# Kernel tuning notes

Measured on AMD Instinct MI355X. Metric: run time of the kernel, lower is better.

The kernel has to match this reference:

```python
import jax, jax.numpy as jnp
import numpy as np

D_MODEL = 1024
D_INNER = 2048   # expand_factor * d_model
D_STATE = 16
D_CONV = 4
DT_RANK = 64     # ceil(d_model / 16)
EPS = 1e-5


def setup_inputs() -> dict:
    key = jax.random.key(0)
    ks = jax.random.split(key, 10)
    B, L = 2, 1024
    w = lambda k, shape, s: (jax.random.normal(k, shape, jnp.float32) * s)
    A = jnp.tile(jnp.arange(1, D_STATE + 1, dtype=jnp.float32), (D_INNER, 1))
    return {
        "hidden_states": jax.random.normal(ks[0], (B, L, D_MODEL), jnp.float32),
        "norm_w": jnp.ones((D_MODEL,), jnp.float32),
        "norm_b": jnp.zeros((D_MODEL,), jnp.float32),
        "in_proj_w": w(ks[1], (D_MODEL, 2 * D_INNER), 0.02),
        "conv_w": w(ks[2], (D_INNER, D_CONV), 0.2),
        "conv_b": jnp.zeros((D_INNER,), jnp.float32),
        "x_proj_w": w(ks[3], (D_INNER, DT_RANK + 2 * D_STATE), 0.02),
        "dt_proj_w": w(ks[4], (DT_RANK, D_INNER), 0.1),
        "dt_proj_b": w(ks[5], (D_INNER,), 0.1),
        "A_log": jnp.log(A),
        "D_param": jnp.ones((D_INNER,), jnp.float32),
        "out_proj_w": w(ks[6], (D_INNER, D_MODEL), 0.02),
    }


def _causal_depthwise_conv(x, conv_w, conv_b):
    # x: [B, L, d_inner] -> causal depthwise conv, kernel size D_CONV
    B, L, C = x.shape
    xt = jnp.transpose(x, (0, 2, 1))                 # [B, C, L]
    xt = jnp.pad(xt, ((0, 0), (0, 0), (D_CONV - 1, 0)))  # left pad == torch pad+truncate
    k = conv_w[:, None, :]                            # [C, 1, K] (OIH, groups=C)
    y = jax.lax.conv_general_dilated(
        xt, k, window_strides=(1,), padding="VALID",
        dimension_numbers=("NCH", "OIH", "NCH"), feature_group_count=C)
    y = y + conv_b[None, :, None]
    return jnp.transpose(y, (0, 2, 1))                # [B, L, C]


def _selective_scan(u, delta, A, Bm, Cm, D_param):
    # u, delta: [B, L, d_inner]; A: [d_inner, d_state]; Bm, Cm: [B, L, d_state]
    dA = jnp.exp(delta[..., None] * A[None, None])            # [B,L,d,n]
    dBu = delta[..., None] * Bm[:, :, None, :] * u[..., None]  # [B,L,d,n]
    h0 = jnp.zeros((u.shape[0], u.shape[2], A.shape[1]), u.dtype)

    def step(h, inp):
        dA_t, dBu_t, c_t = inp          # [B,d,n], [B,d,n], [B,n]
        h = dA_t * h + dBu_t
        y = jnp.einsum("bdn,bn->bd", h, c_t)
        return h, y

    xs = (jnp.moveaxis(dA, 1, 0), jnp.moveaxis(dBu, 1, 0), jnp.moveaxis(Cm, 1, 0))
    _, ys = jax.lax.scan(step, h0, xs)   # ys: [L, B, d]
    y = jnp.moveaxis(ys, 0, 1)           # [B, L, d]
    return y + u * D_param[None, None]


def reference(hidden_states, norm_w, norm_b, in_proj_w, conv_w, conv_b,
              x_proj_w, dt_proj_w, dt_proj_b, A_log, D_param, out_proj_w):
    h = hidden_states
    mu = jnp.mean(h, axis=-1, keepdims=True)
    var = jnp.mean(jnp.square(h - mu), axis=-1, keepdims=True)
    h = (h - mu) * jax.lax.rsqrt(var + EPS) * norm_w + norm_b

    xz = h @ in_proj_w                       # [B,L,2*d_inner]
    x, z = jnp.split(xz, 2, axis=-1)
    x = _causal_depthwise_conv(x, conv_w, conv_b)
    x = jax.nn.silu(x)

    A = -jnp.exp(A_log)                      # [d_inner, d_state]
    xp = x @ x_proj_w                        # [B,L,dt_rank+2*d_state]
    dt_r = xp[..., :DT_RANK]
    Bm = xp[..., DT_RANK:DT_RANK + D_STATE]
    Cm = xp[..., DT_RANK + D_STATE:]
    delta = jax.nn.softplus(dt_r @ dt_proj_w + dt_proj_b)  # [B,L,d_inner]

    y = _selective_scan(x, delta, A, Bm, Cm, D_param)
    y = y * jax.nn.silu(z)
    return y @ out_proj_w
```

## Files before the change

kernel.cpp:

```cpp
#include <hip/hip_runtime.h>
#include <hip/hip_bf16.h>

#define D_MODEL 1024
#define D_INNER 2048
#define D_STATE 16
#define DT_RANK 64
#define NB 2
#define LSEQ 1024
#define NROWS (NB * LSEQ)
#define XPN 96
#define NC 32
#define CL 32

typedef __attribute__((ext_vector_type(8))) short bf16x8;
typedef __attribute__((ext_vector_type(4))) float f32x4;

__device__ __forceinline__ unsigned short f2bf(float x) {
    __hip_bfloat16 h = __float2bfloat16(x);
    return *reinterpret_cast<unsigned short*>(&h);
}
__device__ __forceinline__ float bf2f(unsigned short u) {
    unsigned int v = ((unsigned int)u) << 16;
    float f;
    __builtin_memcpy(&f, &v, 4);
    return f;
}
__device__ __forceinline__ unsigned short f2h(float x) {
    _Float16 h = (_Float16)x;
    unsigned short u;
    __builtin_memcpy(&u, &h, 2);
    return u;
}
__device__ __forceinline__ float h2f(unsigned short u) {
    _Float16 h;
    __builtin_memcpy(&h, &u, 2);
    return (float)h;
}

__global__ __launch_bounds__(256) void wcast_ln(const float* __restrict__ W0, unsigned short* __restrict__ D0,
                                                const float* __restrict__ W1, unsigned short* __restrict__ D1,
                                                const float* __restrict__ W2, unsigned short* __restrict__ D2,
                                                const float* __restrict__ W3, unsigned short* __restrict__ D3,
                                                const float* __restrict__ hx, const float* __restrict__ nw,
                                                const float* __restrict__ nb, unsigned short* __restrict__ lnout) {
    int bid = blockIdx.x;
    if (bid >= 6528) {
        int row = bid - 6528;
        const float4* xr = (const float4*)(hx + (size_t)row * D_MODEL);
        float4 v = xr[threadIdx.x];
        float s = v.x + v.y + v.z + v.w;
        float sq = v.x * v.x + v.y * v.y + v.z * v.z + v.w * v.w;
#pragma unroll
        for (int off = 32; off > 0; off >>= 1) {
            s += __shfl_down(s, off);
            sq += __shfl_down(sq, off);
        }
        __shared__ float ws[4], wq[4];
        __shared__ float smu, srstd;
        int wave = threadIdx.x >> 6;
        if ((threadIdx.x & 63) == 0) { ws[wave] = s; wq[wave] = sq; }
        __syncthreads();
        if (threadIdx.x == 0) {
            float ts = ws[0] + ws[1] + ws[2] + ws[3];
            float tq = wq[0] + wq[1] + wq[2] + wq[3];
            float mu = ts * (1.f / D_MODEL);
            float var = tq * (1.f / D_MODEL) - mu * mu;
            smu = mu;
            srstd = rsqrtf(var + 1e-5f);
        }
        __syncthreads();
        float mu = smu, rstd = srstd;
        float4 wv = ((const float4*)nw)[threadIdx.x];
        float4 bv = ((const float4*)nb)[threadIdx.x];
        ushort4 pk;
        pk.x = f2bf((v.x - mu) * rstd * wv.x + bv.x);
        pk.y = f2bf((v.y - mu) * rstd * wv.y + bv.y);
        pk.z = f2bf((v.z - mu) * rstd * wv.z + bv.z);
        pk.w = f2bf((v.w - mu) * rstd * wv.w + bv.w);
        *(ushort4*)(lnout + (size_t)row * D_MODEL + threadIdx.x * 4) = pk;
        return;
    }
    const float* W;
    unsigned short* Dst;
    int K, Nreal, bx, by;
    if (bid < 4096) { W = W0; Dst = D0; K = 1024; Nreal = 4096; bx = bid & 127; by = bid >> 7; }
    else if (bid < 4352) { int j = bid - 4096; W = W1; Dst = D1; K = 2048; Nreal = 96; bx = j & 3; by = j >> 2; }
    else if (bid < 6400) { int j = bid - 4352; W = W2; Dst = D2; K = 2048; Nreal = 1024; bx = j & 31; by = j >> 5; }
    else { int j = bid - 6400; W = W3; Dst = D3; K = 64; Nreal = 2048; bx = j & 63; by = j >> 6; }
    __shared__ float t[32][33];
    int tn = bx * 32, tk = by * 32;
    for (int e = threadIdx.x; e < 1024; e += 256) {
        int r = e >> 5, c = e & 31;
        int n = tn + c;
        t[r][c] = (n < Nreal) ? W[(size_t)(tk + r) * Nreal + n] : 0.f;
    }
    __syncthreads();
    for (int e = threadIdx.x; e < 1024; e += 256) {
        int r = e >> 5, c = e & 31;
        Dst[(size_t)(tn + r) * K + tk + c] = f2bf(t[c][r]);
    }
}

template <int EPI>
__global__ __launch_bounds__(256) void gemm_bf16(const unsigned short* __restrict__ A,
                                                 const unsigned short* __restrict__ Bt,
                                                 const float* __restrict__ bias,
                                                 float* __restrict__ C,
                                                 void* __restrict__ C2,
                                                 int M, int K, int ldc, int Nreal) {
    __shared__ unsigned short As[128 * 64];
    __shared__ unsigned short Bs[128 * 64];
    int nwg = gridDim.x * gridDim.y;
    int orig = blockIdx.y * gridDim.x + blockIdx.x;
    int q = nwg >> 3, r = nwg & 7;
    int xcd = orig & 7, idx = orig >> 3;
    int newid = (xcd < r ? xcd * (q + 1) : r * (q + 1) + (xcd - r) * q) + idx;
    int bx = newid % gridDim.x, by = newid / gridDim.x;

    int tid = threadIdx.x;
    int lane = tid & 63;
    int wave = tid >> 6;
    int wr = (wave >> 1) * 64, wc = (wave & 1) * 64;
    int bm = by * 128, bn = bx * 128;
    int kchunk = K / gridDim.z;
    int kbeg = blockIdx.z * kchunk;

    f32x4 acc[4][4];
#pragma unroll
    for (int i = 0; i < 4; ++i)
#pragma unroll
        for (int j = 0; j < 4; ++j) acc[i][j] = (f32x4){0.f, 0.f, 0.f, 0.f};

    int ar = lane & 15;
    int kq = lane >> 4;

    for (int k0 = kbeg; k0 < kbeg + kchunk; k0 += 64) {
        __syncthreads();
#pragma unroll
        for (int s = 0; s < 4; ++s) {
            int seg = s * 256 + tid;
            int row = seg >> 3, p = seg & 7;
            int c = p ^ (row & 7);
            __builtin_amdgcn_global_load_lds(
                (const __attribute__((address_space(1))) void*)(A + (size_t)(bm + row) * K + k0 + c * 8),
                (__attribute__((address_space(3))) void*)(As + seg * 8), 16, 0, 0);
        }
#pragma unroll
        for (int s = 0; s < 4; ++s) {
            int seg = s * 256 + tid;
            int row = seg >> 3, p = seg & 7;
            int c = p ^ (row & 7);
            __builtin_amdgcn_global_load_lds(
                (const __attribute__((address_space(1))) void*)(Bt + (size_t)(bn + row) * K + k0 + c * 8),
                (__attribute__((address_space(3))) void*)(Bs + seg * 8), 16, 0, 0);
        }
        __syncthreads();
#pragma unroll
        for (int kk = 0; kk < 2; ++kk) {
            bf16x8 af[4], bfr[4];
#pragma unroll
            for (int i = 0; i < 4; ++i) {
                int row = wr + i * 16 + ar;
                int pos = ((kk << 2) | kq) ^ (row & 7);
                af[i] = *(const bf16x8*)&As[(size_t)row * 64 + pos * 8];
            }
#pragma unroll
            for (int j = 0; j < 4; ++j) {
                int row = wc + j * 16 + ar;
                int pos = ((kk << 2) | kq) ^ (row & 7);
                bfr[j] = *(const bf16x8*)&Bs[(size_t)row * 64 + pos * 8];
            }
#pragma unroll
            for (int i = 0; i < 4; ++i)
#pragma unroll
                for (int j = 0; j < 4; ++j)
                    acc[i][j] = __builtin_amdgcn_mfma_f32_16x16x32_bf16(af[i], bfr[j], acc[i][j], 0, 0, 0);
        }
    }

    int crow0 = bm + wr + (lane >> 4) * 4;
    int ccol0 = bn + wc + (lane & 15);
    size_t zoff = (size_t)blockIdx.z * (size_t)M * ldc;
#pragma unroll
    for (int i = 0; i < 4; ++i)
#pragma unroll
        for (int j = 0; j < 4; ++j) {
            int col = ccol0 + j * 16;
            if (EPI == 0) {
                if (col < Nreal) {
                    float* cp = C + zoff + (size_t)(crow0 + i * 16) * ldc + col;
#pragma unroll
                    for (int rr = 0; rr < 4; ++rr) cp[(size_t)rr * ldc] = acc[i][j][rr];
                }
            } else if (EPI == 2) {
                unsigned short* cx = (unsigned short*)C;
                unsigned short* cz = (unsigned short*)C2;
                if (col < 2048) {
#pragma unroll
                    for (int rr = 0; rr < 4; ++rr)
                        cx[(size_t)(crow0 + i * 16 + rr) * 2048 + col] = f2bf(acc[i][j][rr]);
                } else {
#pragma unroll
                    for (int rr = 0; rr < 4; ++rr)
                        cz[(size_t)(crow0 + i * 16 + rr) * 2048 + (col - 2048)] = f2bf(acc[i][j][rr]);
                }
            } else if (EPI == 3) {
                unsigned short* cp = (unsigned short*)C2 + zoff + (size_t)(crow0 + i * 16) * ldc + col;
#pragma unroll
                for (int rr = 0; rr < 4; ++rr) cp[(size_t)rr * ldc] = f2h(acc[i][j][rr]);
            } else {
                float bv = bias[col];
                unsigned short* cp = (unsigned short*)C2 + (size_t)(crow0 + i * 16) * ldc + col;
#pragma unroll
                for (int rr = 0; rr < 4; ++rr) {
                    float v = acc[i][j][rr] + bv;
                    v = (v > 20.f) ? v : log1pf(__expf(v));
                    cp[(size_t)rr * ldc] = f2bf(v);
                }
            }
        }
}

__global__ __launch_bounds__(256) void reduce_xp(const float* __restrict__ part,
                                                 float* __restrict__ xp,
                                                 unsigned short* __restrict__ dtr) {
    int t = blockIdx.x * 256 + threadIdx.x;
    float s = 0.f;
#pragma unroll
    for (int k = 0; k < 16; ++k) s += part[(size_t)k * ((size_t)NROWS * XPN) + t];
    xp[t] = s;
    int row = t / 96, col = t - row * 96;
    if (col < 64) dtr[(size_t)row * 64 + col] = f2bf(s);
}

__global__ __launch_bounds__(256) void reduce_out(const unsigned short* __restrict__ part,
                                                  float* __restrict__ out) {
    int t = blockIdx.x * 256 + threadIdx.x;
    const size_t stride = (size_t)NROWS * D_MODEL;
    ushort4 p0 = ((const ushort4*)part)[t];
    ushort4 p1 = ((const ushort4*)(part + stride))[t];
    ushort4 p2 = ((const ushort4*)(part + 2 * stride))[t];
    ushort4 p3 = ((const ushort4*)(part + 3 * stride))[t];
    float4 o;
    o.x = h2f(p0.x) + h2f(p1.x) + h2f(p2.x) + h2f(p3.x);
    o.y = h2f(p0.y) + h2f(p1.y) + h2f(p2.y) + h2f(p3.y);
    o.z = h2f(p0.z) + h2f(p1.z) + h2f(p2.z) + h2f(p3.z);
    o.w = h2f(p0.w) + h2f(p1.w) + h2f(p2.w) + h2f(p3.w);
    ((float4*)out)[t] = o;
}

__global__ __launch_bounds__(256) void conv_silu_kernel(const unsigned short* __restrict__ xx,
                                                        const float* __restrict__ cw,
                                                        const float* __restrict__ cb,
                                                        unsigned short* __restrict__ outb) {
    int gid = blockIdx.x * 256 + threadIdx.x;
    int d4 = (gid & 511) << 2;
    int bl = gid >> 9;
    int l = bl & (LSEQ - 1);
    const unsigned short* base = xx + (size_t)bl * D_INNER + d4;
    ushort4 zr4 = {0, 0, 0, 0};
    ushort4 X0 = *(const ushort4*)base;
    ushort4 X1 = (l >= 1) ? *(const ushort4*)(base - D_INNER) : zr4;
    ushort4 X2 = (l >= 2) ? *(const ushort4*)(base - 2 * D_INNER) : zr4;
    ushort4 X3 = (l >= 3) ? *(const ushort4*)(base - 3 * D_INNER) : zr4;
    float4 bias = *(const float4*)(cb + d4);
    const float4* wv = (const float4*)(cw + (size_t)d4 * 4);
    float xs0[4] = {bf2f(X0.x), bf2f(X0.y), bf2f(X0.z), bf2f(X0.w)};
    float xs1[4] = {bf2f(X1.x), bf2f(X1.y), bf2f(X1.z), bf2f(X1.w)};
    float xs2[4] = {bf2f(X2.x), bf2f(X2.y), bf2f(X2.z), bf2f(X2.w)};
    float xs3[4] = {bf2f(X3.x), bf2f(X3.y), bf2f(X3.z), bf2f(X3.w)};
    float bs[4] = {bias.x, bias.y, bias.z, bias.w};
    ushort4 ob;
    unsigned short* obp = (unsigned short*)&ob;
#pragma unroll
    for (int e = 0; e < 4; ++e) {
        float4 we = wv[e];
        float acc = bs[e];
        acc = fmaf(we.w, xs0[e], acc);
        acc = fmaf(we.z, xs1[e], acc);
        acc = fmaf(we.y, xs2[e], acc);
        acc = fmaf(we.x, xs3[e], acc);
        obp[e] = f2bf(acc / (1.f + __expf(-acc)));
    }
    *(ushort4*)(outb + (size_t)bl * D_INNER + d4) = ob;
}

__global__ __launch_bounds__(256) void scan_local(const float* __restrict__ xp,
                                                  const unsigned short* __restrict__ delta,
                                                  const unsigned short* __restrict__ ub,
                                                  const float* __restrict__ A_log,
                                                  float* __restrict__ hst,
                                                  float* __restrict__ sdel) {
    int bc = blockIdx.x >> 3;
    int b = bc >> 5, c = bc & (NC - 1);
    int d = (blockIdx.x & 7) * 256 + threadIdx.x;
    int base_r = b * LSEQ + c * CL;
    __shared__ float Bsm[CL * 16];
    for (int e = threadIdx.x; e < CL * 16; e += 256) {
        int l = e >> 4, n = e & 15;
        Bsm[e] = xp[(size_t)(base_r + l) * XPN + DT_RANK + n];
    }
    __syncthreads();
    float Av[16];
    const float4* ap = (const float4*)(A_log + (size_t)d * 16);
#pragma unroll
    for (int qq = 0; qq < 4; ++qq) {
        float4 a = ap[qq];
        Av[4 * qq + 0] = -__expf(a.x); Av[4 * qq + 1] = -__expf(a.y);
        Av[4 * qq + 2] = -__expf(a.z); Av[4 * qq + 3] = -__expf(a.w);
    }
    float h[16] = {};
    float sd = 0.f;
    const unsigned short* dp = delta + (size_t)base_r * D_INNER + d;
    const unsigned short* up = ub + (size_t)base_r * D_INNER + d;
#pragma unroll 4
    for (int l = 0; l < CL; ++l) {
        float dv = bf2f(dp[(size_t)l * D_INNER]);
        float u = bf2f(up[(size_t)l * D_INNER]);
        float du = dv * u;
        sd += dv;
#pragma unroll
        for (int n = 0; n < 16; ++n) {
            float dA = __expf(dv * Av[n]);
            h[n] = fmaf(dA, h[n], du * Bsm[l * 16 + n]);
        }
    }
    size_t hi = ((size_t)(c * NB + b) * D_INNER + d) * 16;
#pragma unroll
    for (int qq = 0; qq < 4; ++qq) {
        float4 v = make_float4(h[4 * qq], h[4 * qq + 1], h[4 * qq + 2], h[4 * qq + 3]);
        *(float4*)(hst + hi + 4 * qq) = v;
    }
    sdel[(size_t)(c * NB + b) * D_INNER + d] = sd;
}

__global__ __launch_bounds__(256) void scan_combine(const float* __restrict__ A_log,
                                                    const float* __restrict__ sdel,
                                                    float* __restrict__ hst) {
    int t = blockIdx.x * 256 + threadIdx.x;
    int n = t & 15, d = (t >> 4) & (D_INNER - 1), b = t >> 15;
    float Avn = -__expf(A_log[(size_t)d * 16 + n]);
    float h = 0.f;
#pragma unroll 4
    for (int c = 0; c < NC; ++c) {
        size_t base = (size_t)(c * NB + b) * D_INNER + d;
        float* hp = hst + base * 16 + n;
        float S = sdel[base];
        float tmp = *hp;
        *hp = h;
        h = fmaf(__expf(Avn * S), h, tmp);
    }
}

__global__ __launch_bounds__(256) void scan_final(const float* __restrict__ xp,
                                                  const unsigned short* __restrict__ delta,
                                                  const unsigned short* __restrict__ ub,
                                                  const unsigned short* __restrict__ zb,
                                                  const float* __restrict__ hst,
                                                  const float* __restrict__ A_log,
                                                  const float* __restrict__ Dp,
                                                  unsigned short* __restrict__ yb) {
    int bc = blockIdx.x >> 3;
    int b = bc >> 5, c = bc & (NC - 1);
    int d = (blockIdx.x & 7) * 256 + threadIdx.x;
    int base_r = b * LSEQ + c * CL;
    __shared__ float Bsm[CL * 16], Csm[CL * 16];
    for (int e = threadIdx.x; e < CL * 16; e += 256) {
        int l = e >> 4, n = e & 15;
        Bsm[e] = xp[(size_t)(base_r + l) * XPN + DT_RANK + n];
        Csm[e] = xp[(size_t)(base_r + l) * XPN + DT_RANK + 16 + n];
    }
    __syncthreads();
    float Av[16];
    const float4* ap = (const float4*)(A_log + (size_t)d * 16);
#pragma unroll
    for (int qq = 0; qq < 4; ++qq) {
        float4 a = ap[qq];
        Av[4 * qq + 0] = -__expf(a.x); Av[4 * qq + 1] = -__expf(a.y);
        Av[4 * qq + 2] = -__expf(a.z); Av[4 * qq + 3] = -__expf(a.w);
    }
    float h[16];
    size_t hi = ((size_t)(c * NB + b) * D_INNER + d) * 16;
#pragma unroll
    for (int qq = 0; qq < 4; ++qq) {
        float4 v = *(const float4*)(hst + hi + 4 * qq);
        h[4 * qq] = v.x; h[4 * qq + 1] = v.y; h[4 * qq + 2] = v.z; h[4 * qq + 3] = v.w;
    }
    float Dv = Dp[d];
    const unsigned short* dp = delta + (size_t)base_r * D_INNER + d;
    const unsigned short* up = ub + (size_t)base_r * D_INNER + d;
    const unsigned short* zp = zb + (size_t)base_r * D_INNER + d;
#pragma unroll 4
    for (int l = 0; l < CL; ++l) {
        float dv = bf2f(dp[(size_t)l * D_INNER]);
        float u = bf2f(up[(size_t)l * D_INNER]);
        float du = dv * u;
        float acc = 0.f;
#pragma unroll
        for (int n = 0; n < 16; ++n) {
            float dA = __expf(dv * Av[n]);
            h[n] = fmaf(dA, h[n], du * Bsm[l * 16 + n]);
            acc = fmaf(h[n], Csm[l * 16 + n], acc);
        }
        float yv = fmaf(u, Dv, acc);
        float zv = bf2f(zp[(size_t)l * D_INNER]);
        float sz = zv / (1.f + __expf(-zv));
        yb[(size_t)(base_r + l) * D_INNER + d] = f2bf(yv * sz);
    }
}

extern "C" void kernel_launch(void* const* d_in, const int* in_sizes, int n_in,
                              void* d_out, int out_size, void* d_ws, size_t ws_size,
                              hipStream_t stream) {
    const float* hidden = (const float*)d_in[0];
    const float* norm_w = (const float*)d_in[1];
    const float* norm_b = (const float*)d_in[2];
    const float* in_proj_w = (const float*)d_in[3];
    const float* conv_w = (const float*)d_in[4];
    const float* conv_b = (const float*)d_in[5];
    const float* x_proj_w = (const float*)d_in[6];
    const float* dt_proj_w = (const float*)d_in[7];
    const float* dt_proj_b = (const float*)d_in[8];
    const float* A_log = (const float*)d_in[9];
    const float* D_param = (const float*)d_in[10];
    const float* out_proj_w = (const float*)d_in[11];
    float* out = (float*)d_out;

    float* wsf = (float*)d_ws;
    unsigned short* hbufb = (unsigned short*)wsf;
    float* xpbuf = wsf;
    float* sdelbuf = wsf + 196608;
    unsigned short* xb = (unsigned short*)(wsf + 1048576);
    float* hst = wsf + 1048576;
    unsigned short* zb = (unsigned short*)(wsf + 3145728);
    unsigned short* ub = (unsigned short*)(wsf + 5242880);
    unsigned short* yb = ub;
    unsigned short* wAt = (unsigned short*)(wsf + 7340032);
    float* xpart = wsf + 7340032;
    unsigned short* opart = (unsigned short*)(wsf + 7340032);
    unsigned short* wXt = (unsigned short*)(wsf + 10485760);
    unsigned short* wDt = (unsigned short*)(wsf + 10616832);
    unsigned short* dtrb = (unsigned short*)(wsf + 10682368);
    unsigned short* deltab = (unsigned short*)(wsf + 11665408);
    unsigned short* wOt = (unsigned short*)(wsf + 13762560);

    wcast_ln<<<6528 + NROWS, 256, 0, stream>>>(in_proj_w, wAt, x_proj_w, wXt, out_proj_w, wOt,
                                               dt_proj_w, wDt, hidden, norm_w, norm_b, hbufb);

    gemm_bf16<2><<<dim3(4096 / 128, NROWS / 128, 1), 256, 0, stream>>>(
        hbufb, wAt, nullptr, (float*)xb, zb, NROWS, 1024, 2048, 4096);

    conv_silu_kernel<<<(NROWS * D_INNER) / 1024, 256, 0, stream>>>(xb, conv_w, conv_b, ub);

    gemm_bf16<0><<<dim3(1, NROWS / 128, 16), 256, 0, stream>>>(
        ub, wXt, nullptr, xpart, nullptr, NROWS, 2048, XPN, XPN);

    reduce_xp<<<(NROWS * XPN) / 256, 256, 0, stream>>>(xpart, xpbuf, dtrb);

    gemm_bf16<4><<<dim3(D_INNER / 128, NROWS / 128, 1), 256, 0, stream>>>(
        dtrb, wDt, dt_proj_b, nullptr, deltab, NROWS, 64, D_INNER, D_INNER);

    scan_local<<<NB * NC * (D_INNER / 256), 256, 0, stream>>>(
        xpbuf, deltab, ub, A_log, hst, sdelbuf);
    scan_combine<<<(NB * D_INNER * D_STATE) / 256, 256, 0, stream>>>(
        A_log, sdelbuf, hst);
    scan_final<<<NB * NC * (D_INNER / 256), 256, 0, stream>>>(
        xpbuf, deltab, ub, zb, hst, A_log, D_param, yb);

    gemm_bf16<3><<<dim3(1024 / 128, NROWS / 128, 4), 256, 0, stream>>>(
        yb, wOt, nullptr, nullptr, opart, NROWS, 2048, 1024, 1024);

    reduce_out<<<(NROWS * D_MODEL / 4) / 256, 256, 0, stream>>>(opart, out);
}
```

Baseline: 168.0 us.

## Store x_proj split-K partials in fp16 and stage scan combine through LDS

The x_proj split-K GEMM now writes fp16 partials through the EPI 3 epilogue, with an added column bound check, instead of fp32. This halves the traffic for the partial write and for the reduce_xp read. scan_combine is restructured so each block loads all chunk states for 16 channels into shared memory, runs the serial chunk recurrence there, and writes back coalesced. B and C loads in the scan kernels use float4 vectors. The fp16 partials lose precision and risk overflow in the x_proj result.

Measured after the change: 166.9 us. Within noise of the previous version (-0.7%).

```diff
diff --git a/kernel.cpp b/kernel.cpp
--- a/kernel.cpp
+++ b/kernel.cpp
@@ -205,9 +205,11 @@
                         cz[(size_t)(crow0 + i * 16 + rr) * 2048 + (col - 2048)] = f2bf(acc[i][j][rr]);
                 }
             } else if (EPI == 3) {
-                unsigned short* cp = (unsigned short*)C2 + zoff + (size_t)(crow0 + i * 16) * ldc + col;
-#pragma unroll
-                for (int rr = 0; rr < 4; ++rr) cp[(size_t)rr * ldc] = f2h(acc[i][j][rr]);
+                if (col < Nreal) {
+                    unsigned short* cp = (unsigned short*)C2 + zoff + (size_t)(crow0 + i * 16) * ldc + col;
+#pragma unroll
+                    for (int rr = 0; rr < 4; ++rr) cp[(size_t)rr * ldc] = f2h(acc[i][j][rr]);
+                }
             } else {
                 float bv = bias[col];
                 unsigned short* cp = (unsigned short*)C2 + (size_t)(crow0 + i * 16) * ldc + col;
@@ -221,13 +223,13 @@
         }
 }
 
-__global__ __launch_bounds__(256) void reduce_xp(const float* __restrict__ part,
+__global__ __launch_bounds__(256) void reduce_xp(const unsigned short* __restrict__ part,
                                                  float* __restrict__ xp,
                                                  unsigned short* __restrict__ dtr) {
     int t = blockIdx.x * 256 + threadIdx.x;
     float s = 0.f;
 #pragma unroll
-    for (int k = 0; k < 16; ++k) s += part[(size_t)k * ((size_t)NROWS * XPN) + t];
+    for (int k = 0; k < 16; ++k) s += h2f(part[(size_t)k * ((size_t)NROWS * XPN) + t]);
     xp[t] = s;
     int row = t / 96, col = t - row * 96;
     if (col < 64) dtr[(size_t)row * 64 + col] = f2bf(s);
@@ -296,9 +298,10 @@
     int d = (blockIdx.x & 7) * 256 + threadIdx.x;
     int base_r = b * LSEQ + c * CL;
     __shared__ float Bsm[CL * 16];
-    for (int e = threadIdx.x; e < CL * 16; e += 256) {
-        int l = e >> 4, n = e & 15;
-        Bsm[e] = xp[(size_t)(base_r + l) * XPN + DT_RANK + n];
+    for (int e = threadIdx.x; e < CL * 4; e += 256) {
+        int l = e >> 2, q4 = e & 3;
+        float4 v = *(const float4*)&xp[(size_t)(base_r + l) * XPN + DT_RANK + q4 * 4];
+        *(float4*)&Bsm[l * 16 + q4 * 4] = v;
     }
     __syncthreads();
     float Av[16];
@@ -337,18 +340,34 @@
 __global__ __launch_bounds__(256) void scan_combine(const float* __restrict__ A_log,
                                                     const float* __restrict__ sdel,
                                                     float* __restrict__ hst) {
-    int t = blockIdx.x * 256 + threadIdx.x;
-    int n = t & 15, d = (t >> 4) & (D_INNER - 1), b = t >> 15;
-    float Avn = -__expf(A_log[(size_t)d * 16 + n]);
+    __shared__ float hl[NC][256];
+    __shared__ float sl[NC][16];
+    int b = blockIdx.x >> 7;
+    int d0 = (blockIdx.x & 127) * 16;
+    int t = threadIdx.x;
+    int dd = t >> 4;
+    for (int e = t; e < NC * 256; e += 256) {
+        int c = e >> 8, tt = e & 255;
+        hl[c][tt] = hst[(size_t)(c * NB + b) * (D_INNER * 16) + d0 * 16 + tt];
+    }
+    for (int e = t; e < NC * 16; e += 256) {
+        int c = e >> 4, ddd = e & 15;
+        sl[c][ddd] = sdel[(size_t)(c * NB + b) * D_INNER + d0 + ddd];
+    }
+    __syncthreads();
+    float Avn = -__expf(A_log[(size_t)d0 * 16 + t]);
     float h = 0.f;
-#pragma unroll 4
+#pragma unroll
     for (int c = 0; c < NC; ++c) {
-        size_t base = (size_t)(c * NB + b) * D_INNER + d;
-        float* hp = hst + base * 16 + n;
-        float S = sdel[base];
-        float tmp = *hp;
-        *hp = h;
+        float S = sl[c][dd];
+        float tmp = hl[c][t];
+        hl[c][t] = h;
         h = fmaf(__expf(Avn * S), h, tmp);
+    }
+    __syncthreads();
+    for (int e = t; e < NC * 256; e += 256) {
+        int c = e >> 8, tt = e & 255;
+        hst[(size_t)(c * NB + b) * (D_INNER * 16) + d0 * 16 + tt] = hl[c][tt];
     }
 }
 
@@ -365,10 +384,11 @@
     int d = (blockIdx.x & 7) * 256 + threadIdx.x;
     int base_r = b * LSEQ + c * CL;
     __shared__ float Bsm[CL * 16], Csm[CL * 16];
-    for (int e = threadIdx.x; e < CL * 16; e += 256) {
-        int l = e >> 4, n = e & 15;
-        Bsm[e] = xp[(size_t)(base_r + l) * XPN + DT_RANK + n];
-        Csm[e] = xp[(size_t)(base_r + l) * XPN + DT_RANK + 16 + n];
+    for (int e = threadIdx.x; e < CL * 8; e += 256) {
+        int l = e >> 3, q8 = e & 7;
+        float4 v = *(const float4*)&xp[(size_t)(base_r + l) * XPN + DT_RANK + q8 * 4];
+        if (q8 < 4) *(float4*)&Bsm[l * 16 + q8 * 4] = v;
+        else *(float4*)&Csm[l * 16 + (q8 - 4) * 4] = v;
     }
     __syncthreads();
     float Av[16];
@@ -436,7 +456,7 @@
     unsigned short* ub = (unsigned short*)(wsf + 5242880);
     unsigned short* yb = ub;
     unsigned short* wAt = (unsigned short*)(wsf + 7340032);
-    float* xpart = wsf + 7340032;
+    unsigned short* xpart16 = (unsigned short*)(wsf + 7340032);
     unsigned short* opart = (unsigned short*)(wsf + 7340032);
     unsigned short* wXt = (unsigned short*)(wsf + 10485760);
     unsigned short* wDt = (unsigned short*)(wsf + 10616832);
@@ -452,18 +472,17 @@
 
     conv_silu_kernel<<<(NROWS * D_INNER) / 1024, 256, 0, stream>>>(xb, conv_w, conv_b, ub);
 
-    gemm_bf16<0><<<dim3(1, NROWS / 128, 16), 256, 0, stream>>>(
-        ub, wXt, nullptr, xpart, nullptr, NROWS, 2048, XPN, XPN);
-
-    reduce_xp<<<(NROWS * XPN) / 256, 256, 0, stream>>>(xpart, xpbuf, dtrb);
+    gemm_bf16<3><<<dim3(1, NROWS / 128, 16), 256, 0, stream>>>(
+        ub, wXt, nullptr, nullptr, xpart16, NROWS, 2048, XPN, XPN);
+
+    reduce_xp<<<(NROWS * XPN) / 256, 256, 0, stream>>>(xpart16, xpbuf, dtrb);
 
     gemm_bf16<4><<<dim3(D_INNER / 128, NROWS / 128, 1), 256, 0, stream>>>(
         dtrb, wDt, dt_proj_b, nullptr, deltab, NROWS, 64, D_INNER, D_INNER);
 
     scan_local<<<NB * NC * (D_INNER / 256), 256, 0, stream>>>(
         xpbuf, deltab, ub, A_log, hst, sdelbuf);
-    scan_combine<<<(NB * D_INNER * D_STATE) / 256, 256, 0, stream>>>(
-        A_log, sdelbuf, hst);
+    scan_combine<<<256, 256, 0, stream>>>(A_log, sdelbuf, hst);
     scan_final<<<NB * NC * (D_INNER / 256), 256, 0, stream>>>(
         xpbuf, deltab, ub, zb, hst, A_log, D_param, yb);
 
```
